# Kernel optimization log

Hardware: AMD Instinct MI355X
Metric: run time of the kernel (lower is better)

## Reference

```python
import jax, jax.numpy as jnp
import numpy as np

DIM, NH, NKV, HD = 4096, 32, 8, 128
B, KV_LEN, WINDOW = 32, 4096, 4096
G = NH // NKV  # q heads per kv head (GQA group)


def setup_inputs() -> dict:
    key = jax.random.key(0)
    ks = jax.random.split(key, 7)
    s = 1.0 / np.sqrt(DIM)
    return {
        "x": jax.random.normal(ks[0], (1, 1, B, DIM), jnp.float32),
        "wqkv": jax.random.normal(ks[1], (DIM, DIM + 2 * NKV * HD), jnp.float32) * s,
        "wo": jax.random.normal(ks[2], (DIM, DIM), jnp.float32) * s,
        "rot_mat": jax.random.normal(ks[3], (HD, HD), jnp.float32) * (1.0 / np.sqrt(HD)),
        "cache_k": jax.random.normal(ks[4], (B, NKV, KV_LEN, HD), jnp.float32),
        "cache_v": jax.random.normal(ks[5], (B, NKV, KV_LEN, HD), jnp.float32),
        "attn_mask": jnp.zeros((1, NH, B, WINDOW), jnp.float32),
        "current_pos": 4095,
    }


def reference(x, wqkv, wo, rot_mat, cache_k, cache_v, attn_mask, current_pos):
    # fused QKV projection: (1,1,B,DIM) @ (DIM,6144) -> (1,1,B,6144)
    xqkv = x @ wqkv
    q = xqkv[..., : NH * HD].reshape(1, 1, B, NH, HD)
    k = xqkv[..., NH * HD : (NH + NKV) * HD].reshape(1, 1, B, NKV, HD)
    v = xqkv[..., (NH + NKV) * HD :].reshape(1, 1, B, NKV, HD)
    # nlp_create_qkv_heads layout: (seq, n_heads, batch, head_dim)
    q = jnp.transpose(q[:, 0], (0, 2, 1, 3))  # (1, NH, B, HD)
    k = jnp.transpose(k[:, 0], (0, 2, 1, 3))  # (1, NKV, B, HD)
    v = jnp.transpose(v[:, 0], (0, 2, 1, 3))  # (1, NKV, B, HD)
    # RoPE as matmul on last dim
    q = q @ rot_mat
    k = k @ rot_mat
    # KV-cache update at current_pos: cache is (B, NKV, KV_LEN, HD)
    cache_k = cache_k.at[:, :, current_pos, :].set(jnp.transpose(k[0], (1, 0, 2)))
    cache_v = cache_v.at[:, :, current_pos, :].set(jnp.transpose(v[0], (1, 0, 2)))
    # unpad valid region (padded to nearest 32, capped by sliding window)
    L = min(((current_pos + 1 + 31) // 32) * 32, WINDOW)
    keys = cache_k[:, :, :L]    # (B, NKV, L, HD)
    values = cache_v[:, :, :L]  # (B, NKV, L, HD)
    # grouped attention: q (1, NKV, G, B, HD) vs keys (B, NKV, L, HD)
    qg = q.reshape(1, NKV, G, B, HD)
    scores = jnp.einsum("qkgbd,bkld->qkgbl", qg, keys)  # (1,NKV,G,B,L)
    scores = scores.reshape(1, NH, B, L) / jnp.sqrt(jnp.float32(HD))
    scores = scores + attn_mask[..., :L]
    probs = jax.nn.softmax(scores, axis=-1)
    out = jnp.einsum("qkgbl,bkld->qkgbd", probs.reshape(1, NKV, G, B, L), values)
    out = out.reshape(1, NH, B, HD)
    # concatenate heads -> (1,1,B,DIM)
    out = jnp.transpose(out, (0, 2, 1, 3)).reshape(1, 1, B, NH * HD)
    return out @ wo
```

## Files before the change

kernel.cpp:

```cpp
#include <hip/hip_runtime.h>

#define BB 32
#define DIM 4096
#define NH 32
#define NKV 8
#define HD 128
#define KVLEN 4096
#define QKVC 6144
#define GQ 4
#define QKV_SPLITS 32
#define WO_SPLITS 32

__global__ __launch_bounds__(256, 4) void k_qkv(const float* __restrict__ x,
                                                const float* __restrict__ w,
                                                float* __restrict__ part) {
    int j  = blockIdx.x * 256 + threadIdx.x;
    int d0 = blockIdx.y * (DIM / QKV_SPLITS);
    float acc[BB];
#pragma unroll
    for (int b = 0; b < BB; ++b) acc[b] = 0.f;
    for (int dd = d0; dd < d0 + DIM / QKV_SPLITS; dd += 8) {
        float wr[8];
#pragma unroll
        for (int k = 0; k < 8; ++k) wr[k] = w[(size_t)(dd + k) * QKVC + j];
#pragma unroll
        for (int b = 0; b < BB; ++b) {
            float4 xa = *(const float4*)&x[b * DIM + dd];
            float4 xb = *(const float4*)&x[b * DIM + dd + 4];
            float t = acc[b];
            t = fmaf(xa.x, wr[0], t); t = fmaf(xa.y, wr[1], t);
            t = fmaf(xa.z, wr[2], t); t = fmaf(xa.w, wr[3], t);
            t = fmaf(xb.x, wr[4], t); t = fmaf(xb.y, wr[5], t);
            t = fmaf(xb.z, wr[6], t); t = fmaf(xb.w, wr[7], t);
            acc[b] = t;
        }
    }
#pragma unroll
    for (int b = 0; b < BB; ++b)
        part[(size_t)blockIdx.y * (BB * QKVC) + (size_t)b * QKVC + j] = acc[b];
}

__global__ __launch_bounds__(256) void k_red(const float* __restrict__ src,
                                             float* __restrict__ dst,
                                             int parts, int n4) {
    int i = blockIdx.x * 256 + threadIdx.x;
    if (i >= n4) return;
    const float4* s4 = (const float4*)src;
    float4 a = s4[i];
    for (int p = 1; p < parts; ++p) {
        float4 b = s4[(size_t)p * n4 + i];
        a.x += b.x; a.y += b.y; a.z += b.z; a.w += b.w;
    }
    ((float4*)dst)[i] = a;
}

__global__ __launch_bounds__(128) void k_rot(const float* __restrict__ xqkv,
                                             const float* __restrict__ rot,
                                             float* __restrict__ qws,
                                             float* __restrict__ kws) {
    int c  = blockIdx.x;
    int b  = blockIdx.y;
    int dp = threadIdx.x;
    const float* row = &xqkv[(size_t)b * QKVC + c * HD];
    float acc = 0.f;
#pragma unroll 4
    for (int d = 0; d < HD; ++d) acc = fmaf(row[d], rot[d * HD + dp], acc);
    if (c < 32) {
        qws[((size_t)b * NH + c) * HD + dp] = acc;
    } else {
        int kvh = c - 32;
        kws[((size_t)b * NKV + kvh) * HD + dp] = acc;
    }
}

__global__ __launch_bounds__(256, 4) void k_attn(const float* __restrict__ ck,
                                                 const float* __restrict__ cv,
                                                 const float* __restrict__ qws,
                                                 const float* __restrict__ kws,
                                                 const float* __restrict__ xqkv,
                                                 const float* __restrict__ mask,
                                                 const int* __restrict__ curpos,
                                                 float* __restrict__ opart,
                                                 float2* __restrict__ stats) {
    __shared__ float Kl[64 * 132];
    __shared__ float ql[GQ * HD];
    __shared__ float pl[GQ * 64];
    __shared__ float rs[GQ];
    int bkv = blockIdx.x;
    int split = blockIdx.y;
    int b = bkv >> 3, kv = bkv & 7;
    int tid = threadIdx.x;
    int g = tid >> 6, lane = tid & 63;
    int d4 = tid & 31, sub = tid >> 5;
    int pos = *curpos;
    int L = min((((pos + 1) + 31) >> 5) << 5, KVLEN);
    int l0 = split * 1024;
    int h = kv * GQ + g;
    const float scale = 0.08838834764831845f;

    for (int i = tid; i < GQ * HD; i += 256)
        ql[i] = qws[((size_t)b * NH + kv * GQ) * HD + i];

    const float4 vnew4 = *(const float4*)&xqkv[(size_t)b * QKVC + (NH + NKV) * HD + kv * HD + d4 * 4];

    const float4* Kbase = (const float4*)&ck[((size_t)bkv * KVLEN + l0) * HD];
    const float4* Vbase = (const float4*)&cv[((size_t)bkv * KVLEN + l0) * HD];
    float4 kreg[8], vreg[8];
#pragma unroll
    for (int i = 0; i < 8; ++i) kreg[i] = Kbase[i * 256 + tid];
#pragma unroll
    for (int i = 0; i < 8; ++i) vreg[i] = Vbase[(size_t)(sub * 8 + i) * 32 + d4];

    float m = -3.0e38f, lsum = 0.f;
    float4 acc[GQ];
#pragma unroll
    for (int gg = 0; gg < GQ; ++gg) acc[gg] = make_float4(0.f, 0.f, 0.f, 0.f);

    for (int t = 0; t < 16; ++t) {
#pragma unroll
        for (int i = 0; i < 8; ++i) {
            int c4i = i * 256 + tid;
            int row = c4i >> 5, c4 = c4i & 31;
            *(float4*)&Kl[row * 132 + c4 * 4] = kreg[i];
        }
        int prow = pos - (l0 + t * 64);
        if (prow >= 0 && prow < 64 && tid < 32)
            *(float4*)&Kl[prow * 132 + tid * 4] =
                *(const float4*)&kws[((size_t)b * NKV + kv) * HD + tid * 4];
        __syncthreads();
        if (t < 15) {
            const float4* Kn = Kbase + (size_t)(t + 1) * 2048;
#pragma unroll
            for (int i = 0; i < 8; ++i) kreg[i] = Kn[i * 256 + tid];
        }
        int l = l0 + t * 64 + lane;
        float mk = mask[((size_t)h * BB + b) * KVLEN + l];
        float s = 0.f;
#pragma unroll
        for (int dd = 0; dd < 32; ++dd) {
            float4 kk = *(const float4*)&Kl[lane * 132 + dd * 4];
            float4 qq = *(const float4*)&ql[g * HD + dd * 4];
            s += kk.x * qq.x + kk.y * qq.y + kk.z * qq.z + kk.w * qq.w;
        }
        s = s * scale + mk;
        if (l >= L) s = -3.0e38f;
        float smax = s;
#pragma unroll
        for (int off = 32; off > 0; off >>= 1)
            smax = fmaxf(smax, __shfl_xor(smax, off));
        float mnew = fmaxf(m, smax);
        float r = __expf(m - mnew);
        float e = (l < L) ? __expf(s - mnew) : 0.f;
        float esum = e;
#pragma unroll
        for (int off = 32; off > 0; off >>= 1)
            esum += __shfl_xor(esum, off);
        lsum = lsum * r + esum;
        m = mnew;
        pl[g * 64 + lane] = e;
        if (lane == 0) rs[g] = r;
        __syncthreads();
        float rg;
#pragma unroll
        for (int gg = 0; gg < GQ; ++gg) {
            rg = rs[gg];
            acc[gg].x *= rg; acc[gg].y *= rg;
            acc[gg].z *= rg; acc[gg].w *= rg;
        }
        int vrow = prow - sub * 8;
        if (prow >= 0 && prow < 64) {
#pragma unroll
            for (int i = 0; i < 8; ++i) {
                float4 v = (i == vrow) ? vnew4 : vreg[i];
#pragma unroll
                for (int gg = 0; gg < GQ; ++gg) {
                    float p = pl[gg * 64 + sub * 8 + i];
                    acc[gg].x = fmaf(p, v.x, acc[gg].x);
                    acc[gg].y = fmaf(p, v.y, acc[gg].y);
                    acc[gg].z = fmaf(p, v.z, acc[gg].z);
                    acc[gg].w = fmaf(p, v.w, acc[gg].w);
                }
            }
        } else {
#pragma unroll
            for (int i = 0; i < 8; ++i) {
                float4 v = vreg[i];
#pragma unroll
                for (int gg = 0; gg < GQ; ++gg) {
                    float p = pl[gg * 64 + sub * 8 + i];
                    acc[gg].x = fmaf(p, v.x, acc[gg].x);
                    acc[gg].y = fmaf(p, v.y, acc[gg].y);
                    acc[gg].z = fmaf(p, v.z, acc[gg].z);
                    acc[gg].w = fmaf(p, v.w, acc[gg].w);
                }
            }
        }
        if (t < 15) {
            const float4* Vn = Vbase + (size_t)(t + 1) * 2048;
#pragma unroll
            for (int i = 0; i < 8; ++i)
                vreg[i] = Vn[(size_t)(sub * 8 + i) * 32 + d4];
        }
    }
    if (lane == 0) stats[(bkv * GQ + g) * 4 + split] = make_float2(m, lsum);

    float* red = Kl;
#pragma unroll
    for (int gg = 0; gg < GQ; ++gg)
        *(float4*)&red[(sub * GQ + gg) * HD + d4 * 4] = acc[gg];
    __syncthreads();
#pragma unroll
    for (int rep = 0; rep < 2; ++rep) {
        int idx = rep * 256 + tid;
        int g2 = idx >> 7, d = idx & 127;
        float o = 0.f;
#pragma unroll
        for (int k = 0; k < 8; ++k) o += red[(k * GQ + g2) * HD + d];
        opart[(((size_t)split * 256 + bkv) * GQ + g2) * HD + d] = o;
    }
}

__global__ __launch_bounds__(128) void k_merge(const float* __restrict__ opart,
                                               const float2* __restrict__ stats,
                                               float* __restrict__ attn) {
    int bkv = blockIdx.x;
    int d = threadIdx.x;
    int b = bkv >> 3, kv = bkv & 7;
#pragma unroll
    for (int g = 0; g < GQ; ++g) {
        float2 st[4];
        float M = -3.0e38f;
#pragma unroll
        for (int s = 0; s < 4; ++s) {
            st[s] = stats[(bkv * GQ + g) * 4 + s];
            M = fmaxf(M, st[s].x);
        }
        float Ltot = 0.f;
        float w[4];
#pragma unroll
        for (int s = 0; s < 4; ++s) {
            w[s] = __expf(st[s].x - M);
            Ltot += st[s].y * w[s];
        }
        float inv = Ltot > 0.f ? 1.f / Ltot : 0.f;
        float o = 0.f;
#pragma unroll
        for (int s = 0; s < 4; ++s)
            o += opart[(((size_t)s * 256 + bkv) * GQ + g) * HD + d] * (w[s] * inv);
        attn[(size_t)b * DIM + (kv * GQ + g) * HD + d] = o;
    }
}

__global__ __launch_bounds__(256, 4) void k_wo(const float* __restrict__ attn,
                                               const float* __restrict__ wo,
                                               float* __restrict__ part) {
    int j  = blockIdx.x * 256 + threadIdx.x;
    int d0 = blockIdx.y * (DIM / WO_SPLITS);
    float acc[BB];
#pragma unroll
    for (int b = 0; b < BB; ++b) acc[b] = 0.f;
    for (int dd = d0; dd < d0 + DIM / WO_SPLITS; dd += 8) {
        float wr[8];
#pragma unroll
        for (int k = 0; k < 8; ++k) wr[k] = wo[(size_t)(dd + k) * DIM + j];
#pragma unroll
        for (int b = 0; b < BB; ++b) {
            float4 xa = *(const float4*)&attn[b * DIM + dd];
            float4 xb = *(const float4*)&attn[b * DIM + dd + 4];
            float t = acc[b];
            t = fmaf(xa.x, wr[0], t); t = fmaf(xa.y, wr[1], t);
            t = fmaf(xa.z, wr[2], t); t = fmaf(xa.w, wr[3], t);
            t = fmaf(xb.x, wr[4], t); t = fmaf(xb.y, wr[5], t);
            t = fmaf(xb.z, wr[6], t); t = fmaf(xb.w, wr[7], t);
            acc[b] = t;
        }
    }
#pragma unroll
    for (int b = 0; b < BB; ++b)
        part[(size_t)blockIdx.y * (BB * DIM) + (size_t)b * DIM + j] = acc[b];
}

extern "C" void kernel_launch(void* const* d_in, const int* in_sizes, int n_in,
                              void* d_out, int out_size, void* d_ws, size_t ws_size,
                              hipStream_t stream) {
    const float* x    = (const float*)d_in[0];
    const float* wqkv = (const float*)d_in[1];
    const float* wo   = (const float*)d_in[2];
    const float* rot  = (const float*)d_in[3];
    const float* ck   = (const float*)d_in[4];
    const float* cv   = (const float*)d_in[5];
    const float* mask = (const float*)d_in[6];
    const int* curpos = (const int*)d_in[7];
    float* out        = (float*)d_out;

    char* ws = (char*)d_ws;
    float*  xqkv_part = (float*)(ws);
    float*  xqkv      = (float*)(ws + 25165824);
    float*  qws       = (float*)(ws + 25952256);
    float*  kws       = (float*)(ws + 26476544);
    float*  opart     = (float*)(ws + 26607616);
    float2* stats     = (float2*)(ws + 28704768);
    float*  attn      = (float*)(ws + 28737536);
    float*  out_part  = (float*)(ws + 29261824);

    k_qkv  <<<dim3(QKVC / 256, QKV_SPLITS), 256, 0, stream>>>(x, wqkv, xqkv_part);
    k_red  <<<dim3(192),                    256, 0, stream>>>(xqkv_part, xqkv, QKV_SPLITS, BB * QKVC / 4);
    k_rot  <<<dim3(40, BB),                 128, 0, stream>>>(xqkv, rot, qws, kws);
    k_attn <<<dim3(BB * NKV, 4),            256, 0, stream>>>(ck, cv, qws, kws, xqkv, mask, curpos, opart, stats);
    k_merge<<<dim3(BB * NKV),               128, 0, stream>>>(opart, stats, attn);
    k_wo   <<<dim3(DIM / 256, WO_SPLITS),   256, 0, stream>>>(attn, wo, out_part);
    k_red  <<<dim3(128),                    256, 0, stream>>>(out_part, out, WO_SPLITS, BB * DIM / 4);
}
```

Measured before the change: 1.396 ms.

## Rewrite attention as per-wave direct-load split-KV with more splits

The attention kernel drops the shared-memory K staging and block-wide synchronisation. Each 64-lane wave now handles one query head and reads K rows directly from global memory, with each lane loading a full 128-float row. It broadcasts probabilities via shuffles for the PV step and reads V as float2 per lane. The KV length is split 8 ways instead of 4, the launch bound targets higher occupancy, and the merge kernel and workspace offsets are updated to match. This removes barriers and shared-memory traffic, but each of the four waves in a block now reloads the same K/V rows, and the per-lane strided K row reads are uncoalesced, so the kernel relies on cache reuse.

```diff
diff --git a/kernel.cpp b/kernel.cpp
--- a/kernel.cpp
+++ b/kernel.cpp
@@ -10,6 +10,7 @@
 #define GQ 4
 #define QKV_SPLITS 32
 #define WO_SPLITS 32
+#define ASPLIT 8
 
 __global__ __launch_bounds__(256, 4) void k_qkv(const float* __restrict__ x,
                                                 const float* __restrict__ w,
@@ -73,7 +74,7 @@
     }
 }
 
-__global__ __launch_bounds__(256, 4) void k_attn(const float* __restrict__ ck,
+__global__ __launch_bounds__(256, 8) void k_attn(const float* __restrict__ ck,
                                                  const float* __restrict__ cv,
                                                  const float* __restrict__ qws,
                                                  const float* __restrict__ kws,
@@ -82,142 +83,69 @@
                                                  const int* __restrict__ curpos,
                                                  float* __restrict__ opart,
                                                  float2* __restrict__ stats) {
-    __shared__ float Kl[64 * 132];
-    __shared__ float ql[GQ * HD];
-    __shared__ float pl[GQ * 64];
-    __shared__ float rs[GQ];
+    __shared__ float ql[GQ][HD];
     int bkv = blockIdx.x;
     int split = blockIdx.y;
     int b = bkv >> 3, kv = bkv & 7;
     int tid = threadIdx.x;
     int g = tid >> 6, lane = tid & 63;
-    int d4 = tid & 31, sub = tid >> 5;
     int pos = *curpos;
     int L = min((((pos + 1) + 31) >> 5) << 5, KVLEN);
-    int l0 = split * 1024;
+    int l0 = split * 512;
     int h = kv * GQ + g;
     const float scale = 0.08838834764831845f;
 
-    for (int i = tid; i < GQ * HD; i += 256)
-        ql[i] = qws[((size_t)b * NH + kv * GQ) * HD + i];
-
-    const float4 vnew4 = *(const float4*)&xqkv[(size_t)b * QKVC + (NH + NKV) * HD + kv * HD + d4 * 4];
-
-    const float4* Kbase = (const float4*)&ck[((size_t)bkv * KVLEN + l0) * HD];
-    const float4* Vbase = (const float4*)&cv[((size_t)bkv * KVLEN + l0) * HD];
-    float4 kreg[8], vreg[8];
-#pragma unroll
-    for (int i = 0; i < 8; ++i) kreg[i] = Kbase[i * 256 + tid];
-#pragma unroll
-    for (int i = 0; i < 8; ++i) vreg[i] = Vbase[(size_t)(sub * 8 + i) * 32 + d4];
+    *(float2*)&ql[g][lane * 2] = *(const float2*)&qws[((size_t)b * NH + h) * HD + lane * 2];
+
+    const float* Kb   = ck + (size_t)bkv * KVLEN * HD;
+    const float* Vb   = cv + (size_t)bkv * KVLEN * HD;
+    const float* kw   = kws + ((size_t)b * NKV + kv) * HD;
+    const float* vz   = xqkv + (size_t)b * QKVC + (size_t)(NH + NKV) * HD + kv * HD;
+    const float* mrow = mask + ((size_t)h * BB + b) * KVLEN;
 
     float m = -3.0e38f, lsum = 0.f;
-    float4 acc[GQ];
-#pragma unroll
-    for (int gg = 0; gg < GQ; ++gg) acc[gg] = make_float4(0.f, 0.f, 0.f, 0.f);
-
-    for (int t = 0; t < 16; ++t) {
-#pragma unroll
-        for (int i = 0; i < 8; ++i) {
-            int c4i = i * 256 + tid;
-            int row = c4i >> 5, c4 = c4i & 31;
-            *(float4*)&Kl[row * 132 + c4 * 4] = kreg[i];
-        }
-        int prow = pos - (l0 + t * 64);
-        if (prow >= 0 && prow < 64 && tid < 32)
-            *(float4*)&Kl[prow * 132 + tid * 4] =
-                *(const float4*)&kws[((size_t)b * NKV + kv) * HD + tid * 4];
-        __syncthreads();
-        if (t < 15) {
-            const float4* Kn = Kbase + (size_t)(t + 1) * 2048;
-#pragma unroll
-            for (int i = 0; i < 8; ++i) kreg[i] = Kn[i * 256 + tid];
-        }
-        int l = l0 + t * 64 + lane;
-        float mk = mask[((size_t)h * BB + b) * KVLEN + l];
+    float2 acc = make_float2(0.f, 0.f);
+
+    for (int c = 0; c < 8; ++c) {
+        int lk = l0 + c * 64 + lane;
+        const float* krow = (lk == pos) ? kw : (Kb + (size_t)lk * HD);
         float s = 0.f;
 #pragma unroll
-        for (int dd = 0; dd < 32; ++dd) {
-            float4 kk = *(const float4*)&Kl[lane * 132 + dd * 4];
-            float4 qq = *(const float4*)&ql[g * HD + dd * 4];
+        for (int d4 = 0; d4 < 32; ++d4) {
+            float4 kk = *(const float4*)&krow[d4 * 4];
+            float4 qq = *(const float4*)&ql[g][d4 * 4];
             s += kk.x * qq.x + kk.y * qq.y + kk.z * qq.z + kk.w * qq.w;
         }
-        s = s * scale + mk;
-        if (l >= L) s = -3.0e38f;
+        s = s * scale + mrow[lk];
+        if (lk >= L) s = -3.0e38f;
         float smax = s;
 #pragma unroll
         for (int off = 32; off > 0; off >>= 1)
             smax = fmaxf(smax, __shfl_xor(smax, off));
         float mnew = fmaxf(m, smax);
         float r = __expf(m - mnew);
-        float e = (l < L) ? __expf(s - mnew) : 0.f;
+        float e = (lk < L) ? __expf(s - mnew) : 0.f;
         float esum = e;
 #pragma unroll
         for (int off = 32; off > 0; off >>= 1)
             esum += __shfl_xor(esum, off);
         lsum = lsum * r + esum;
         m = mnew;
-        pl[g * 64 + lane] = e;
-        if (lane == 0) rs[g] = r;
-        __syncthreads();
-        float rg;
-#pragma unroll
-        for (int gg = 0; gg < GQ; ++gg) {
-            rg = rs[gg];
-            acc[gg].x *= rg; acc[gg].y *= rg;
-            acc[gg].z *= rg; acc[gg].w *= rg;
-        }
-        int vrow = prow - sub * 8;
-        if (prow >= 0 && prow < 64) {
-#pragma unroll
-            for (int i = 0; i < 8; ++i) {
-                float4 v = (i == vrow) ? vnew4 : vreg[i];
-#pragma unroll
-                for (int gg = 0; gg < GQ; ++gg) {
-                    float p = pl[gg * 64 + sub * 8 + i];
-                    acc[gg].x = fmaf(p, v.x, acc[gg].x);
-                    acc[gg].y = fmaf(p, v.y, acc[gg].y);
-                    acc[gg].z = fmaf(p, v.z, acc[gg].z);
-                    acc[gg].w = fmaf(p, v.w, acc[gg].w);
-                }
-            }
-        } else {
-#pragma unroll
-            for (int i = 0; i < 8; ++i) {
-                float4 v = vreg[i];
-#pragma unroll
-                for (int gg = 0; gg < GQ; ++gg) {
-                    float p = pl[gg * 64 + sub * 8 + i];
-                    acc[gg].x = fmaf(p, v.x, acc[gg].x);
-                    acc[gg].y = fmaf(p, v.y, acc[gg].y);
-                    acc[gg].z = fmaf(p, v.z, acc[gg].z);
-                    acc[gg].w = fmaf(p, v.w, acc[gg].w);
-                }
-            }
-        }
-        if (t < 15) {
-            const float4* Vn = Vbase + (size_t)(t + 1) * 2048;
-#pragma unroll
-            for (int i = 0; i < 8; ++i)
-                vreg[i] = Vn[(size_t)(sub * 8 + i) * 32 + d4];
-        }
-    }
-    if (lane == 0) stats[(bkv * GQ + g) * 4 + split] = make_float2(m, lsum);
-
-    float* red = Kl;
-#pragma unroll
-    for (int gg = 0; gg < GQ; ++gg)
-        *(float4*)&red[(sub * GQ + gg) * HD + d4 * 4] = acc[gg];
-    __syncthreads();
-#pragma unroll
-    for (int rep = 0; rep < 2; ++rep) {
-        int idx = rep * 256 + tid;
-        int g2 = idx >> 7, d = idx & 127;
-        float o = 0.f;
-#pragma unroll
-        for (int k = 0; k < 8; ++k) o += red[(k * GQ + g2) * HD + d];
-        opart[(((size_t)split * 256 + bkv) * GQ + g2) * HD + d] = o;
-    }
+        acc.x *= r; acc.y *= r;
+
+        const float* Vt = Vb + (size_t)(l0 + c * 64) * HD;
+        int prow = pos - (l0 + c * 64);
+#pragma unroll
+        for (int i = 0; i < 64; ++i) {
+            float p = __shfl(e, i);
+            const float* vr = (i == prow) ? vz : (Vt + (size_t)i * HD);
+            float2 v = *(const float2*)&vr[lane * 2];
+            acc.x = fmaf(p, v.x, acc.x);
+            acc.y = fmaf(p, v.y, acc.y);
+        }
+    }
+    if (lane == 0) stats[(bkv * GQ + g) * ASPLIT + split] = make_float2(m, lsum);
+    *(float2*)&opart[(((size_t)split * 256 + bkv) * GQ + g) * HD + lane * 2] = acc;
 }
 
 __global__ __launch_bounds__(128) void k_merge(const float* __restrict__ opart,
@@ -228,24 +156,24 @@
     int b = bkv >> 3, kv = bkv & 7;
 #pragma unroll
     for (int g = 0; g < GQ; ++g) {
-        float2 st[4];
+        float2 st[ASPLIT];
         float M = -3.0e38f;
 #pragma unroll
-        for (int s = 0; s < 4; ++s) {
-            st[s] = stats[(bkv * GQ + g) * 4 + s];
+        for (int s = 0; s < ASPLIT; ++s) {
+            st[s] = stats[(bkv * GQ + g) * ASPLIT + s];
             M = fmaxf(M, st[s].x);
         }
         float Ltot = 0.f;
-        float w[4];
-#pragma unroll
-        for (int s = 0; s < 4; ++s) {
+        float w[ASPLIT];
+#pragma unroll
+        for (int s = 0; s < ASPLIT; ++s) {
             w[s] = __expf(st[s].x - M);
             Ltot += st[s].y * w[s];
         }
         float inv = Ltot > 0.f ? 1.f / Ltot : 0.f;
         float o = 0.f;
 #pragma unroll
-        for (int s = 0; s < 4; ++s)
+        for (int s = 0; s < ASPLIT; ++s)
             o += opart[(((size_t)s * 256 + bkv) * GQ + g) * HD + d] * (w[s] * inv);
         attn[(size_t)b * DIM + (kv * GQ + g) * HD + d] = o;
     }
@@ -299,14 +227,14 @@
     float*  qws       = (float*)(ws + 25952256);
     float*  kws       = (float*)(ws + 26476544);
     float*  opart     = (float*)(ws + 26607616);
-    float2* stats     = (float2*)(ws + 28704768);
-    float*  attn      = (float*)(ws + 28737536);
-    float*  out_part  = (float*)(ws + 29261824);
+    float2* stats     = (float2*)(ws + 30801920);
+    float*  attn      = (float*)(ws + 30867456);
+    float*  out_part  = (float*)(ws + 31391744);
 
     k_qkv  <<<dim3(QKVC / 256, QKV_SPLITS), 256, 0, stream>>>(x, wqkv, xqkv_part);
     k_red  <<<dim3(192),                    256, 0, stream>>>(xqkv_part, xqkv, QKV_SPLITS, BB * QKVC / 4);
     k_rot  <<<dim3(40, BB),                 128, 0, stream>>>(xqkv, rot, qws, kws);
-    k_attn <<<dim3(BB * NKV, 4),            256, 0, stream>>>(ck, cv, qws, kws, xqkv, mask, curpos, opart, stats);
+    k_attn <<<dim3(BB * NKV, ASPLIT),       256, 0, stream>>>(ck, cv, qws, kws, xqkv, mask, curpos, opart, stats);
     k_merge<<<dim3(BB * NKV),               128, 0, stream>>>(opart, stats, attn);
     k_wo   <<<dim3(DIM / 256, WO_SPLITS),   256, 0, stream>>>(attn, wo, out_part);
     k_red  <<<dim3(128),                    256, 0, stream>>>(out_part, out, WO_SPLITS, BB * DIM / 4);
```

Result: slower. 1.850 ms (+32.5%).
